# Kernel optimization log

Measured on AMD Instinct MI355X. Metric: run time of the kernel, lower is better.

Reference implementation:

```python
import jax, jax.numpy as jnp
import numpy as np

THRESH = 0.9
NUM_HEADS = 4
HEAD_DIM = 8


def _ln(x, g, b, eps=1e-5):
    m = x.mean(-1, keepdims=True)
    v = ((x - m) ** 2).mean(-1, keepdims=True)
    return (x - m) * jax.lax.rsqrt(v + eps) * g + b


def setup_inputs() -> dict:
    key = jax.random.key(0)
    ks = jax.random.split(key, 32)
    n, d_in, h1, h2, d, ffn, nb = 4096, 512, 128, 64, 32, 64, 2

    def w(k, shape, fan_in):
        return jax.random.normal(k, shape, jnp.float32) * (1.0 / np.sqrt(fan_in))

    inp = {}
    inp["x"] = jax.random.normal(ks[0], (n, d_in), jnp.float32)
    # Autoencoder encoder: input_dim -> 128 -> 64 -> latent_dim
    inp["enc_w1"] = w(ks[1], (d_in, h1), d_in); inp["enc_b1"] = jnp.zeros((h1,), jnp.float32)
    inp["enc_w2"] = w(ks[2], (h1, h2), h1);     inp["enc_b2"] = jnp.zeros((h2,), jnp.float32)
    inp["enc_w3"] = w(ks[3], (h2, d), h2);      inp["enc_b3"] = jnp.zeros((d,), jnp.float32)
    # Transformer blocks (stacked over num_blocks=2)
    inp["wq"] = w(ks[4], (nb, d, d), d); inp["bq"] = jnp.zeros((nb, d), jnp.float32)
    inp["wk"] = w(ks[5], (nb, d, d), d); inp["bk"] = jnp.zeros((nb, d), jnp.float32)
    inp["wv"] = w(ks[6], (nb, d, d), d); inp["bv"] = jnp.zeros((nb, d), jnp.float32)
    inp["wo"] = w(ks[7], (nb, d, d), d); inp["bo"] = jnp.zeros((nb, d), jnp.float32)
    inp["ln1_g"] = jnp.ones((nb, d), jnp.float32);  inp["ln1_b"] = jnp.zeros((nb, d), jnp.float32)
    inp["ffn_w1"] = w(ks[8], (nb, d, ffn), d);      inp["ffn_b1"] = jnp.zeros((nb, ffn), jnp.float32)
    inp["ffn_w2"] = w(ks[9], (nb, ffn, d), ffn);    inp["ffn_b2"] = jnp.zeros((nb, d), jnp.float32)
    inp["ln2_g"] = jnp.ones((nb, d), jnp.float32);  inp["ln2_b"] = jnp.zeros((nb, d), jnp.float32)
    # Head: Linear(d,16) -> Tanh -> Linear(16, num_classes)
    inp["head_w1"] = w(ks[10], (d, 16), d);  inp["head_b1"] = jnp.zeros((16,), jnp.float32)
    inp["head_w2"] = w(ks[11], (16, 1), 16); inp["head_b2"] = jnp.zeros((1,), jnp.float32)
    return inp


def reference(x, enc_w1, enc_b1, enc_w2, enc_b2, enc_w3, enc_b3,
              wq, bq, wk, bk, wv, bv, wo, bo,
              ln1_g, ln1_b, ffn_w1, ffn_b1, ffn_w2, ffn_b2, ln2_g, ln2_b,
              head_w1, head_b1, head_w2, head_b2):
    # --- autoencoder encode: [n, d_in] -> [n, d] ---
    a = jax.nn.relu(x @ enc_w1 + enc_b1)
    a = jax.nn.relu(a @ enc_w2 + enc_b2)
    latent = a @ enc_w3 + enc_b3  # [n, d]

    # --- graph pool: cosine-sim threshold mask, per-node masked neighbor mean ---
    # self-similarity is 1.0 >= THRESH, so every node has >=1 neighbor (deg>=1)
    norms = jnp.linalg.norm(latent, axis=1, keepdims=True) + 1e-12
    normed = latent / norms
    sims = normed @ normed.T                                  # [n, n]
    mask = (sims >= THRESH).astype(latent.dtype)              # [n, n]
    deg = mask.sum(axis=1, keepdims=True)                     # [n, 1]
    pooled = latent + (mask @ latent) / deg                   # latent[i] + mean of neighbors

    # --- transformer blocks (post-LN, eval mode: dropout off) ---
    h = pooled[None]  # [1, n, d]
    n, d = pooled.shape
    nb = wq.shape[0]
    scale = 1.0 / np.sqrt(HEAD_DIM)
    for i in range(nb):
        q = (h @ wq[i] + bq[i]).reshape(1, n, NUM_HEADS, HEAD_DIM)
        k = (h @ wk[i] + bk[i]).reshape(1, n, NUM_HEADS, HEAD_DIM)
        v = (h @ wv[i] + bv[i]).reshape(1, n, NUM_HEADS, HEAD_DIM)
        scores = jnp.einsum('bqhd,bkhd->bhqk', q, k) * scale  # [1, H, n, n]
        attn = jax.nn.softmax(scores, axis=-1)
        o = jnp.einsum('bhqk,bkhd->bqhd', attn, v).reshape(1, n, d)
        o = o @ wo[i] + bo[i]
        h = _ln(h + o, ln1_g[i], ln1_b[i])
        f = jax.nn.relu(h @ ffn_w1[i] + ffn_b1[i]) @ ffn_w2[i] + ffn_b2[i]
        h = _ln(h + f, ln2_g[i], ln2_b[i])

    # --- head on mean-pooled sequence ---
    m = h.mean(axis=1)  # [1, d]
    out = jnp.tanh(m @ head_w1 + head_b1) @ head_w2 + head_b2  # [1, 1]
    return out.squeeze()
```

## Files before the change

### kernel.cpp

```cpp
#include <hip/hip_runtime.h>
#include <math.h>

#define N 4096
#define DIN 512
#define D 32
#define JC 8

typedef float v2f __attribute__((ext_vector_type(2)));
__device__ __forceinline__ v2f fma2(v2f a, float b, v2f c) {
  v2f bb; bb.x = b; bb.y = b;
  return __builtin_elementwise_fma(a, bb, c);
}

__global__ __launch_bounds__(256) void enc_kernel(
    const float* __restrict__ x,
    const float* __restrict__ w1, const float* __restrict__ b1,
    const float* __restrict__ w2, const float* __restrict__ b2,
    const float* __restrict__ w3, const float* __restrict__ b3,
    float* __restrict__ latent, float* __restrict__ normed) {
  __shared__ float xs[8][512];
  __shared__ float h1p[4][8][128];
  __shared__ float h1s[8][128];
  __shared__ float h2s[8][64];
  __shared__ float w2s[128][64];
  __shared__ float w3s[64][32];
  const int t = threadIdx.x;
  const int r0 = blockIdx.x * 8;

  const float4* xg = (const float4*)(x + (size_t)r0 * DIN);
  float4* xl = (float4*)&xs[0][0];
#pragma unroll
  for (int i = 0; i < 4; ++i) xl[t + i * 256] = xg[t + i * 256];
  float4* w2l = (float4*)&w2s[0][0];
  const float4* w2g = (const float4*)w2;
#pragma unroll
  for (int i = 0; i < 8; ++i) w2l[t + i * 256] = w2g[t + i * 256];
  float4* w3l = (float4*)&w3s[0][0];
  const float4* w3g = (const float4*)w3;
#pragma unroll
  for (int i = 0; i < 2; ++i) w3l[t + i * 256] = w3g[t + i * 256];
  __syncthreads();

  {
    const int jc2 = (t & 63) * 2;
    const int kq = t >> 6;
    const int kb = kq * 128;
    float a0[8], a1[8];
#pragma unroll
    for (int r = 0; r < 8; ++r) { a0[r] = 0.f; a1[r] = 0.f; }
    const float* wp = w1 + (size_t)kb * 128 + jc2;

#define ENC_LD4(P0, P1, P2, P3, KK)                          \
    P0 = *(const float2*)&wp[(size_t)(KK) * 128];            \
    P1 = *(const float2*)&wp[(size_t)((KK) + 1) * 128];      \
    P2 = *(const float2*)&wp[(size_t)((KK) + 2) * 128];      \
    P3 = *(const float2*)&wp[(size_t)((KK) + 3) * 128];

#define ENC_STEP(W0, WA, WB, WC, KK)                                   \
    {                                                                  \
      _Pragma("unroll")                                                \
      for (int r = 0; r < 8; ++r) {                                    \
        const float4 xv = *(const float4*)&xs[r][kb + (KK)];           \
        a0[r] = fmaf(xv.x, W0.x, a0[r]); a1[r] = fmaf(xv.x, W0.y, a1[r]); \
        a0[r] = fmaf(xv.y, WA.x, a0[r]); a1[r] = fmaf(xv.y, WA.y, a1[r]); \
        a0[r] = fmaf(xv.z, WB.x, a0[r]); a1[r] = fmaf(xv.z, WB.y, a1[r]); \
        a0[r] = fmaf(xv.w, WC.x, a0[r]); a1[r] = fmaf(xv.w, WC.y, a1[r]); \
      }                                                                \
    }

    float2 A0, A1, A2, A3, B0, B1, B2, B3, C0, C1, C2, C3, D0, D1, D2, D3;
    ENC_LD4(A0, A1, A2, A3, 0)
    ENC_LD4(B0, B1, B2, B3, 4)
    ENC_LD4(C0, C1, C2, C3, 8)
    ENC_LD4(D0, D1, D2, D3, 12)
    for (int kk = 0; kk < 128; kk += 16) {
      ENC_STEP(A0, A1, A2, A3, kk + 0);
      if (kk + 16 < 128) { ENC_LD4(A0, A1, A2, A3, kk + 16) }
      ENC_STEP(B0, B1, B2, B3, kk + 4);
      if (kk + 20 < 128) { ENC_LD4(B0, B1, B2, B3, kk + 20) }
      ENC_STEP(C0, C1, C2, C3, kk + 8);
      if (kk + 24 < 128) { ENC_LD4(C0, C1, C2, C3, kk + 24) }
      ENC_STEP(D0, D1, D2, D3, kk + 12);
      if (kk + 28 < 128) { ENC_LD4(D0, D1, D2, D3, kk + 28) }
    }
#undef ENC_STEP
#undef ENC_LD4
#pragma unroll
    for (int r = 0; r < 8; ++r) {
      h1p[kq][r][jc2] = a0[r];
      h1p[kq][r][jc2 + 1] = a1[r];
    }
  }
  __syncthreads();

#pragma unroll
  for (int e0 = 0; e0 < 1024; e0 += 256) {
    const int e = e0 + t;
    const int r = e >> 7, c = e & 127;
    const float s = b1[c] + ((h1p[0][r][c] + h1p[1][r][c]) + (h1p[2][r][c] + h1p[3][r][c]));
    h1s[r][c] = fmaxf(s, 0.f);
  }
  __syncthreads();

  {
    const int j = t & 63, rg = t >> 6;
    const int ra = rg * 2, rb = ra + 1;
    float a0 = b2[j], a1 = b2[j];
#pragma unroll 8
    for (int kk = 0; kk < 128; ++kk) {
      const float w = w2s[kk][j];
      a0 = fmaf(h1s[ra][kk], w, a0);
      a1 = fmaf(h1s[rb][kk], w, a1);
    }
    h2s[ra][j] = fmaxf(a0, 0.f);
    h2s[rb][j] = fmaxf(a1, 0.f);
  }
  __syncthreads();

  {
    const int j = t & 31, og = t >> 5;
    float acc = b3[j];
#pragma unroll 8
    for (int kk = 0; kk < 64; ++kk) acc = fmaf(h2s[og][kk], w3s[kk][j], acc);
    float s2 = acc * acc;
    s2 += __shfl_xor(s2, 1);
    s2 += __shfl_xor(s2, 2);
    s2 += __shfl_xor(s2, 4);
    s2 += __shfl_xor(s2, 8);
    s2 += __shfl_xor(s2, 16);
    const float inv = 1.0f / (sqrtf(s2) + 1e-12f);
    const size_t off = (size_t)(r0 + og) * D + j;
    latent[off] = acc;
    normed[off] = acc * inv;
  }
}

__global__ __launch_bounds__(256) __attribute__((amdgpu_waves_per_eu(2, 2)))
void pool_kernel(const float* __restrict__ normed,
                 const float* __restrict__ latent,
                 float* __restrict__ pacc,
                 float* __restrict__ pdeg) {
  __shared__ float smem[8192];
  float* nt = smem;
  float* lt = smem + 4096;
  const int t = threadIdx.x;
  const int jg = t & 7, ip = t >> 3;
  const int i0 = blockIdx.x * 64;
  const int j0 = blockIdx.y * 512;

  v2f nip[32];
  {
    const float* nr0 = normed + (size_t)(i0 + ip) * D;
    const float* nr1 = normed + (size_t)(i0 + ip + 32) * D;
#pragma unroll
    for (int c = 0; c < 32; ++c) { nip[c].x = nr0[c]; nip[c].y = nr1[c]; }
  }

  v2f accp[32], deg2;
#pragma unroll
  for (int c = 0; c < 32; ++c) { accp[c].x = 0.f; accp[c].y = 0.f; }
  deg2.x = 0.f; deg2.y = 0.f;

  for (int jt = j0; jt < j0 + 512; jt += 128) {
    __syncthreads();
    const float4* ng = (const float4*)(normed + (size_t)jt * D);
    const float4* lg = (const float4*)(latent + (size_t)jt * D);
    float4* ntl = (float4*)nt;
    float4* ltl = (float4*)lt;
#pragma unroll
    for (int i = 0; i < 4; ++i) {
      const int gidx = t + i * 256;
      const int r = gidx >> 3, cc = gidx & 7, slot = cc ^ (r & 7);
      ntl[r * 8 + slot] = ng[gidx];
      ltl[r * 8 + slot] = lg[gidx];
    }
    __syncthreads();
#pragma unroll 2
    for (int jj = jg; jj < 128; jj += 8) {
      const float4* nr = (const float4*)nt + jj * 8;
      const int sw = jj & 7;
      v2f s2; s2.x = 0.f; s2.y = 0.f;
#pragma unroll
      for (int c4 = 0; c4 < 8; ++c4) {
        const float4 nv = nr[c4 ^ sw];
        s2 = fma2(nip[c4 * 4 + 0], nv.x, s2);
        s2 = fma2(nip[c4 * 4 + 1], nv.y, s2);
        s2 = fma2(nip[c4 * 4 + 2], nv.z, s2);
        s2 = fma2(nip[c4 * 4 + 3], nv.w, s2);
      }
      if (s2.x >= 0.9f || s2.y >= 0.9f) {
        v2f m2;
        m2.x = (s2.x >= 0.9f) ? 1.f : 0.f;
        m2.y = (s2.y >= 0.9f) ? 1.f : 0.f;
        deg2 += m2;
        const float4* lr = (const float4*)lt + jj * 8;
#pragma unroll
        for (int c4 = 0; c4 < 8; ++c4) {
          const float4 lv = lr[c4 ^ sw];
          accp[c4 * 4 + 0] = fma2(m2, lv.x, accp[c4 * 4 + 0]);
          accp[c4 * 4 + 1] = fma2(m2, lv.y, accp[c4 * 4 + 1]);
          accp[c4 * 4 + 2] = fma2(m2, lv.z, accp[c4 * 4 + 2]);
          accp[c4 * 4 + 3] = fma2(m2, lv.w, accp[c4 * 4 + 3]);
        }
      }
    }
  }
#pragma unroll
  for (int m = 1; m <= 4; m <<= 1) {
#pragma unroll
    for (int c = 0; c < 32; ++c) {
      accp[c].x += __shfl_xor(accp[c].x, m);
      accp[c].y += __shfl_xor(accp[c].y, m);
    }
    deg2.x += __shfl_xor(deg2.x, m);
    deg2.y += __shfl_xor(deg2.y, m);
  }
  if (jg == 0) {
    float* pa0 = pacc + ((size_t)blockIdx.y * N + i0 + ip) * 32;
    float* pa1 = pacc + ((size_t)blockIdx.y * N + i0 + ip + 32) * 32;
#pragma unroll
    for (int c = 0; c < 32; ++c) {
      pa0[c] = accp[c].x;
      pa1[c] = accp[c].y;
    }
    pdeg[(size_t)blockIdx.y * N + i0 + ip] = deg2.x;
    pdeg[(size_t)blockIdx.y * N + i0 + ip + 32] = deg2.y;
  }
}

__global__ __launch_bounds__(256) void pool_combine(const float* __restrict__ latent,
                                                    const float* __restrict__ pacc,
                                                    const float* __restrict__ pdeg,
                                                    float* __restrict__ h) {
  const int e = blockIdx.x * 256 + threadIdx.x;
  const int i = e >> 5;
  float s = 0.f, dg = 0.f;
#pragma unroll
  for (int gch = 0; gch < JC; ++gch) {
    s += pacc[(size_t)gch * N * 32 + e];
    dg += pdeg[(size_t)gch * N + i];
  }
  h[e] = latent[e] + s / dg;
}

__global__ __launch_bounds__(256) void qkv_kernel(
    const float* __restrict__ h,
    const float* __restrict__ wq, const float* __restrict__ bq,
    const float* __restrict__ wk, const float* __restrict__ bk,
    const float* __restrict__ wv, const float* __restrict__ bv,
    float* __restrict__ q, float* __restrict__ k, float* __restrict__ v,
    int* __restrict__ kmax2i) {
  __shared__ float hs[32][32];
  __shared__ float wsm[3][32][32];
  __shared__ int kred[4];
  const int t = threadIdx.x;
  const int r0 = blockIdx.x * 32;
  if (t < 4) kred[t] = 0;
  ((float4*)&hs[0][0])[t] = ((const float4*)(h + (size_t)r0 * 32))[t];
  ((float4*)&wsm[0][0][0])[t] = ((const float4*)wq)[t];
  ((float4*)&wsm[1][0][0])[t] = ((const float4*)wk)[t];
  ((float4*)&wsm[2][0][0])[t] = ((const float4*)wv)[t];
  __syncthreads();
  const int j = t & 31, og = t >> 5;
  const int head = j >> 3;
  float aq[4], ak[4], av[4];
#pragma unroll
  for (int u = 0; u < 4; ++u) { aq[u] = bq[j]; ak[u] = bk[j]; av[u] = bv[j]; }
  for (int kk = 0; kk < 32; ++kk) {
    const float wqv = wsm[0][kk][j], wkv = wsm[1][kk][j], wvv = wsm[2][kk][j];
#pragma unroll
    for (int u = 0; u < 4; ++u) {
      const float hh = hs[og * 4 + u][kk];
      aq[u] = fmaf(hh, wqv, aq[u]);
      ak[u] = fmaf(hh, wkv, ak[u]);
      av[u] = fmaf(hh, wvv, av[u]);
    }
  }
  const float scale = 1.4426950408889634f * 0.35355339059327373f;
#pragma unroll
  for (int u = 0; u < 4; ++u) {
    const size_t off = (size_t)(r0 + og * 4 + u) * 32 + j;
    q[off] = aq[u] * scale;
    k[off] = ak[u];
    v[off] = av[u];
  }
#pragma unroll
  for (int u = 0; u < 4; ++u) {
    float s2 = ak[u] * ak[u];
    s2 += __shfl_xor(s2, 1);
    s2 += __shfl_xor(s2, 2);
    s2 += __shfl_xor(s2, 4);
    if ((j & 7) == 0) atomicMax(&kred[head], __float_as_int(s2));
  }
  __syncthreads();
  if (t < 4) atomicMax(&kmax2i[t], kred[t]);
}

__global__ __launch_bounds__(256, 4)
void attn_kernel(const float* __restrict__ q,
                 const float* __restrict__ k,
                 const float* __restrict__ v,
                 const int* __restrict__ kmax2i,
                 float* __restrict__ apacc,
                 float* __restrict__ apl) {
  __shared__ float4 tiles[1024];
  float4* kls = tiles;
  float4* vls = tiles + 512;
  const int t = threadIdx.x;
  const int jg = t & 7, head = (t >> 3) & 3, rg = t >> 5;
  const int r0 = blockIdx.x * 32;
  const int j0 = blockIdx.y * (N / JC);

  const float km2 = __int_as_float(kmax2i[head]);

  v2f qq[2][8], acc[2][8], mneg2[2], l2[2];
#pragma unroll
  for (int pr = 0; pr < 2; ++pr) {
    const float* qr0 = q + (size_t)(r0 + rg * 4 + 2 * pr) * 32 + head * 8;
    const float* qr1 = qr0 + 32;
    const float4 qa0 = ((const float4*)qr0)[0], qb0 = ((const float4*)qr0)[1];
    const float4 qa1 = ((const float4*)qr1)[0], qb1 = ((const float4*)qr1)[1];
    qq[pr][0].x = qa0.x; qq[pr][0].y = qa1.x;
    qq[pr][1].x = qa0.y; qq[pr][1].y = qa1.y;
    qq[pr][2].x = qa0.z; qq[pr][2].y = qa1.z;
    qq[pr][3].x = qa0.w; qq[pr][3].y = qa1.w;
    qq[pr][4].x = qb0.x; qq[pr][4].y = qb1.x;
    qq[pr][5].x = qb0.y; qq[pr][5].y = qb1.y;
    qq[pr][6].x = qb0.z; qq[pr][6].y = qb1.z;
    qq[pr][7].x = qb0.w; qq[pr][7].y = qb1.w;
    const float qn0 = qa0.x * qa0.x + qa0.y * qa0.y + qa0.z * qa0.z + qa0.w * qa0.w +
                      qb0.x * qb0.x + qb0.y * qb0.y + qb0.z * qb0.z + qb0.w * qb0.w;
    const float qn1 = qa1.x * qa1.x + qa1.y * qa1.y + qa1.z * qa1.z + qa1.w * qa1.w +
                      qb1.x * qb1.x + qb1.y * qb1.y + qb1.z * qb1.z + qb1.w * qb1.w;
    mneg2[pr].x = -sqrtf(qn0 * km2);
    mneg2[pr].y = -sqrtf(qn1 * km2);
    l2[pr].x = 0.f; l2[pr].y = 0.f;
#pragma unroll
    for (int c = 0; c < 8; ++c) { acc[pr][c].x = 0.f; acc[pr][c].y = 0.f; }
  }

  float4 kr0, kr1, vr0, vr1;
  {
    const float4* kg = (const float4*)(k + (size_t)j0 * 32);
    const float4* vg = (const float4*)(v + (size_t)j0 * 32);
    kr0 = kg[t]; kr1 = kg[t + 256];
    vr0 = vg[t]; vr1 = vg[t + 256];
  }

  const int rA = t >> 3, slotA = (t & 7) ^ (rA & 7);
  const int g1 = t + 256;
  const int rB = g1 >> 3, slotB = (g1 & 7) ^ (rB & 7);

  const int h2 = head * 2;
  const int s0 = h2 ^ jg, s1 = (h2 + 1) ^ jg;
  for (int jt = j0; jt < j0 + (N / JC); jt += 64) {
    __syncthreads();
    kls[rA * 8 + slotA] = kr0;
    kls[rB * 8 + slotB] = kr1;
    vls[rA * 8 + slotA] = vr0;
    vls[rB * 8 + slotB] = vr1;
    __syncthreads();
    if (jt + 64 < j0 + (N / JC)) {
      const float4* kg = (const float4*)(k + (size_t)(jt + 64) * 32);
      const float4* vg = (const float4*)(v + (size_t)(jt + 64) * 32);
      kr0 = kg[t]; kr1 = kg[t + 256];
      vr0 = vg[t]; vr1 = vg[t + 256];
    }
#pragma unroll 2
    for (int it = 0; it < 8; ++it) {
      const int jj = it * 8 + jg;
      const float4 ka = kls[jj * 8 + s0];
      const float4 kb = kls[jj * 8 + s1];
      const float4 va = vls[jj * 8 + s0];
      const float4 vb = vls[jj * 8 + s1];
#pragma unroll
      for (int pr = 0; pr < 2; ++pr) {
        v2f s2 = mneg2[pr];
        s2 = fma2(qq[pr][0], ka.x, s2);
        s2 = fma2(qq[pr][1], ka.y, s2);
        s2 = fma2(qq[pr][2], ka.z, s2);
        s2 = fma2(qq[pr][3], ka.w, s2);
        s2 = fma2(qq[pr][4], kb.x, s2);
        s2 = fma2(qq[pr][5], kb.y, s2);
        s2 = fma2(qq[pr][6], kb.z, s2);
        s2 = fma2(qq[pr][7], kb.w, s2);
        v2f p2;
        p2.x = __builtin_amdgcn_exp2f(s2.x);
        p2.y = __builtin_amdgcn_exp2f(s2.y);
        l2[pr] += p2;
        acc[pr][0] = fma2(p2, va.x, acc[pr][0]);
        acc[pr][1] = fma2(p2, va.y, acc[pr][1]);
        acc[pr][2] = fma2(p2, va.z, acc[pr][2]);
        acc[pr][3] = fma2(p2, va.w, acc[pr][3]);
        acc[pr][4] = fma2(p2, vb.x, acc[pr][4]);
        acc[pr][5] = fma2(p2, vb.y, acc[pr][5]);
        acc[pr][6] = fma2(p2, vb.z, acc[pr][6]);
        acc[pr][7] = fma2(p2, vb.w, acc[pr][7]);
      }
    }
  }
#pragma unroll
  for (int pr = 0; pr < 2; ++pr) {
#pragma unroll
    for (int m = 1; m <= 4; m <<= 1) {
#pragma unroll
      for (int c = 0; c < 8; ++c) {
        acc[pr][c].x += __shfl_xor(acc[pr][c].x, m);
        acc[pr][c].y += __shfl_xor(acc[pr][c].y, m);
      }
      l2[pr].x += __shfl_xor(l2[pr].x, m);
      l2[pr].y += __shfl_xor(l2[pr].y, m);
    }
  }
  if (jg == 0) {
    const size_t abase = (size_t)blockIdx.y * N * 32;
    const size_t lbase = (size_t)blockIdx.y * N * 4;
#pragma unroll
    for (int pr = 0; pr < 2; ++pr) {
      const int row0 = r0 + rg * 4 + 2 * pr;
      float* ap0 = apacc + abase + (size_t)row0 * 32 + head * 8;
      float* ap1 = ap0 + 32;
#pragma unroll
      for (int c = 0; c < 8; ++c) {
        ap0[c] = acc[pr][c].x;
        ap1[c] = acc[pr][c].y;
      }
      apl[lbase + (size_t)row0 * 4 + head] = l2[pr].x;
      apl[lbase + (size_t)(row0 + 1) * 4 + head] = l2[pr].y;
    }
  }
}

__global__ __launch_bounds__(256) void acombine(const float* __restrict__ apacc,
                                                const float* __restrict__ apl,
                                                float* __restrict__ attno) {
  const int e = blockIdx.x * 256 + threadIdx.x;
  const int row = e >> 5;
  const int hh = (e >> 3) & 3;
  float L = 0.f, S = 0.f;
#pragma unroll
  for (int jc = 0; jc < JC; ++jc) {
    L += apl[(size_t)jc * N * 4 + row * 4 + hh];
    S += apacc[(size_t)jc * N * 32 + e];
  }
  attno[e] = S / L;
}

__global__ __launch_bounds__(256) void oln1_kernel(const float* __restrict__ attno,
                                                   const float* __restrict__ wo,
                                                   const float* __restrict__ bo,
                                                   const float* __restrict__ g,
                                                   const float* __restrict__ b,
                                                   float* __restrict__ h) {
  __shared__ float als[32][32];
  __shared__ float wols[32][32];
  __shared__ float ys[32][33];
  const int t = threadIdx.x;
  const int r0 = blockIdx.x * 32;
  ((float4*)&als[0][0])[t] = ((const float4*)(attno + (size_t)r0 * 32))[t];
  ((float4*)&wols[0][0])[t] = ((const float4*)wo)[t];
  __syncthreads();
  const int j = t & 31, og = t >> 5;
  float acc[4];
#pragma unroll
  for (int u = 0; u < 4; ++u) acc[u] = bo[j];
  for (int kk = 0; kk < 32; ++kk) {
    const float w = wols[kk][j];
#pragma unroll
    for (int u = 0; u < 4; ++u) acc[u] = fmaf(als[og * 4 + u][kk], w, acc[u]);
  }
#pragma unroll
  for (int u = 0; u < 4; ++u) {
    const int r = og * 4 + u;
    ys[r][j] = h[(size_t)(r0 + r) * 32 + j] + acc[u];
  }
  __syncthreads();
  if (t < 32) {
    float mu = 0.f;
#pragma unroll
    for (int c = 0; c < 32; ++c) mu += ys[t][c];
    mu *= (1.f / 32.f);
    float var = 0.f;
#pragma unroll
    for (int c = 0; c < 32; ++c) {
      const float dd = ys[t][c] - mu;
      var = fmaf(dd, dd, var);
    }
    var *= (1.f / 32.f);
    const float rs = rsqrtf(var + 1e-5f);
#pragma unroll
    for (int c = 0; c < 32; ++c)
      h[(size_t)(r0 + t) * 32 + c] = (ys[t][c] - mu) * rs * g[c] + b[c];
  }
}

__global__ __launch_bounds__(256) void ffn_kernel(const float* __restrict__ hin,
                                                  const float* __restrict__ w1,
                                                  const float* __restrict__ b1,
                                                  const float* __restrict__ w2,
                                                  const float* __restrict__ b2,
                                                  const float* __restrict__ g,
                                                  const float* __restrict__ bb,
                                                  float* __restrict__ h) {
  __shared__ float hs[32][32];
  __shared__ float w1s[32][64];
  __shared__ float w2s[64][32];
  __shared__ float mids[32][64];
  __shared__ float ys[32][33];
  const int t = threadIdx.x;
  const int r0 = blockIdx.x * 32;
  ((float4*)&hs[0][0])[t] = ((const float4*)(hin + (size_t)r0 * 32))[t];
#pragma unroll
  for (int i = 0; i < 2; ++i) {
    ((float4*)&w1s[0][0])[t + i * 256] = ((const float4*)w1)[t + i * 256];
    ((float4*)&w2s[0][0])[t + i * 256] = ((const float4*)w2)[t + i * 256];
  }
  __syncthreads();
  {
    const int jm = t & 63, gg = t >> 6;
    float acc[8];
#pragma unroll
    for (int u = 0; u < 8; ++u) acc[u] = b1[jm];
    for (int kk = 0; kk < 32; ++kk) {
      const float w = w1s[kk][jm];
#pragma unroll
      for (int u = 0; u < 8; ++u) acc[u] = fmaf(hs[gg * 8 + u][kk], w, acc[u]);
    }
#pragma unroll
    for (int u = 0; u < 8; ++u) mids[gg * 8 + u][jm] = fmaxf(acc[u], 0.f);
  }
  __syncthreads();
  {
    const int j = t & 31, og = t >> 5;
    float acc[4];
#pragma unroll
    for (int u = 0; u < 4; ++u) acc[u] = b2[j];
    for (int kk = 0; kk < 64; ++kk) {
      const float w = w2s[kk][j];
#pragma unroll
      for (int u = 0; u < 4; ++u) acc[u] = fmaf(mids[og * 4 + u][kk], w, acc[u]);
    }
#pragma unroll
    for (int u = 0; u < 4; ++u) {
      const int r = og * 4 + u;
      ys[r][j] = hs[r][j] + acc[u];
    }
  }
  __syncthreads();
  if (t < 32) {
    float mu = 0.f;
#pragma unroll
    for (int c = 0; c < 32; ++c) mu += ys[t][c];
    mu *= (1.f / 32.f);
    float var = 0.f;
#pragma unroll
    for (int c = 0; c < 32; ++c) {
      const float dd = ys[t][c] - mu;
      var = fmaf(dd, dd, var);
    }
    var *= (1.f / 32.f);
    const float rs = rsqrtf(var + 1e-5f);
#pragma unroll
    for (int c = 0; c < 32; ++c)
      h[(size_t)(r0 + t) * 32 + c] = (ys[t][c] - mu) * rs * g[c] + bb[c];
  }
}

__global__ __launch_bounds__(256) void headp_kernel(const float* __restrict__ h,
                                                    float* __restrict__ partial) {
  __shared__ float red[8][32];
  const int t = threadIdx.x;
  const int c = t & 31, rg = t >> 5;
  const int r0 = blockIdx.x * 64;
  float s = 0.f;
#pragma unroll
  for (int u = 0; u < 8; ++u) s += h[(size_t)(r0 + rg * 8 + u) * 32 + c];
  red[rg][c] = s;
  __syncthreads();
  if (t < 32) {
    float ss = 0.f;
#pragma unroll
    for (int u = 0; u < 8; ++u) ss += red[u][t];
    partial[blockIdx.x * 32 + t] = ss;
  }
}

__global__ __launch_bounds__(64) void headf_kernel(const float* __restrict__ partial,
                                                   const float* __restrict__ w1,
                                                   const float* __restrict__ b1,
                                                   const float* __restrict__ w2,
                                                   const float* __restrict__ b2,
                                                   float* __restrict__ out) {
  __shared__ float mls[32];
  __shared__ float tls[16];
  const int t = threadIdx.x;
  if (t < 32) {
    float s = 0.f;
    for (int bb = 0; bb < 64; ++bb) s += partial[bb * 32 + t];
    mls[t] = s * (1.f / 4096.f);
  }
  __syncthreads();
  if (t < 16) {
    float a = b1[t];
#pragma unroll
    for (int c = 0; c < 32; ++c) a = fmaf(mls[c], w1[c * 16 + t], a);
    tls[t] = tanhf(a);
  }
  __syncthreads();
  if (t == 0) {
    float o = b2[0];
#pragma unroll
    for (int jj = 0; jj < 16; ++jj) o = fmaf(tls[jj], w2[jj], o);
    out[0] = o;
  }
}

extern "C" void kernel_launch(void* const* d_in, const int* in_sizes, int n_in,
                              void* d_out, int out_size, void* d_ws, size_t ws_size,
                              hipStream_t stream) {
  const float* x      = (const float*)d_in[0];
  const float* enc_w1 = (const float*)d_in[1];
  const float* enc_b1 = (const float*)d_in[2];
  const float* enc_w2 = (const float*)d_in[3];
  const float* enc_b2 = (const float*)d_in[4];
  const float* enc_w3 = (const float*)d_in[5];
  const float* enc_b3 = (const float*)d_in[6];
  const float* wq     = (const float*)d_in[7];
  const float* bq     = (const float*)d_in[8];
  const float* wk     = (const float*)d_in[9];
  const float* bk     = (const float*)d_in[10];
  const float* wv     = (const float*)d_in[11];
  const float* bv     = (const float*)d_in[12];
  const float* wo     = (const float*)d_in[13];
  const float* bo     = (const float*)d_in[14];
  const float* ln1_g  = (const float*)d_in[15];
  const float* ln1_b  = (const float*)d_in[16];
  const float* ffn_w1 = (const float*)d_in[17];
  const float* ffn_b1 = (const float*)d_in[18];
  const float* ffn_w2 = (const float*)d_in[19];
  const float* ffn_b2 = (const float*)d_in[20];
  const float* ln2_g  = (const float*)d_in[21];
  const float* ln2_b  = (const float*)d_in[22];
  const float* head_w1 = (const float*)d_in[23];
  const float* head_b1 = (const float*)d_in[24];
  const float* head_w2 = (const float*)d_in[25];
  const float* head_b2 = (const float*)d_in[26];

  float* ws      = (float*)d_ws;
  float* latent  = ws;
  float* normed  = ws + 131072;
  float* h       = ws + 262144;
  float* q       = ws + 393216;
  float* k       = ws + 524288;
  float* v       = ws + 655360;
  float* attno   = ws + 786432;
  float* shreg   = ws + 917504;
  float* p_acc   = shreg;
  float* p_deg   = shreg + 1048576;
  float* a_acc   = shreg;
  float* a_l     = shreg + 1048576;
  int*   kmax2i  = (int*)(ws + 2097152);
  float* partial = ws + 2097216;

  hipMemsetAsync(kmax2i, 0, 8 * sizeof(int), stream);

  enc_kernel<<<512, 256, 0, stream>>>(x, enc_w1, enc_b1, enc_w2, enc_b2, enc_w3, enc_b3,
                                      latent, normed);
  pool_kernel<<<dim3(64, JC), 256, 0, stream>>>(normed, latent, p_acc, p_deg);
  pool_combine<<<512, 256, 0, stream>>>(latent, p_acc, p_deg, h);

  for (int blk = 0; blk < 2; ++blk) {
    qkv_kernel<<<128, 256, 0, stream>>>(h, wq + blk * 1024, bq + blk * 32,
                                        wk + blk * 1024, bk + blk * 32,
                                        wv + blk * 1024, bv + blk * 32, q, k, v,
                                        kmax2i + blk * 4);
    attn_kernel<<<dim3(128, JC), 256, 0, stream>>>(q, k, v, kmax2i + blk * 4, a_acc, a_l);
    acombine<<<512, 256, 0, stream>>>(a_acc, a_l, attno);
    oln1_kernel<<<128, 256, 0, stream>>>(attno, wo + blk * 1024, bo + blk * 32,
                                         ln1_g + blk * 32, ln1_b + blk * 32, h);
    ffn_kernel<<<128, 256, 0, stream>>>(h, ffn_w1 + blk * 2048, ffn_b1 + blk * 64,
                                        ffn_w2 + blk * 2048, ffn_b2 + blk * 32,
                                        ln2_g + blk * 32, ln2_b + blk * 32, h);
  }

  headp_kernel<<<64, 256, 0, stream>>>(h, partial);
  headf_kernel<<<1, 64, 0, stream>>>(partial, head_w1, head_b1, head_w2, head_b2, (float*)d_out);
}
```

Baseline: 171.6 us.

## Fuse split-K combine steps and output-proj/LN/FFN into neighboring kernels

Folds the pooling partial-sum combine into the first qkv kernel, and folds the attention partial combine, the output projection with LN1, and the FFN with LN2 into a single kernel per block. This removes several small launches and the global round trips through the attno and h intermediates. In exchange the fused kernel uses more shared memory per block, which may lower occupancy, and qkv gains a runtime branch.

```diff
diff --git a/kernel.cpp b/kernel.cpp
--- a/kernel.cpp
+++ b/kernel.cpp
@@ -228,35 +228,45 @@
   }
 }
 
-__global__ __launch_bounds__(256) void pool_combine(const float* __restrict__ latent,
-                                                    const float* __restrict__ pacc,
-                                                    const float* __restrict__ pdeg,
-                                                    float* __restrict__ h) {
-  const int e = blockIdx.x * 256 + threadIdx.x;
-  const int i = e >> 5;
-  float s = 0.f, dg = 0.f;
-#pragma unroll
-  for (int gch = 0; gch < JC; ++gch) {
-    s += pacc[(size_t)gch * N * 32 + e];
-    dg += pdeg[(size_t)gch * N + i];
-  }
-  h[e] = latent[e] + s / dg;
-}
-
 __global__ __launch_bounds__(256) void qkv_kernel(
-    const float* __restrict__ h,
+    float* __restrict__ h,
     const float* __restrict__ wq, const float* __restrict__ bq,
     const float* __restrict__ wk, const float* __restrict__ bk,
     const float* __restrict__ wv, const float* __restrict__ bv,
     float* __restrict__ q, float* __restrict__ k, float* __restrict__ v,
-    int* __restrict__ kmax2i) {
+    int* __restrict__ kmax2i,
+    const float* __restrict__ latent,
+    const float* __restrict__ pacc,
+    const float* __restrict__ pdeg,
+    int fuse_combine) {
   __shared__ float hs[32][32];
   __shared__ float wsm[3][32][32];
   __shared__ int kred[4];
   const int t = threadIdx.x;
   const int r0 = blockIdx.x * 32;
   if (t < 4) kred[t] = 0;
-  ((float4*)&hs[0][0])[t] = ((const float4*)(h + (size_t)r0 * 32))[t];
+  if (fuse_combine) {
+    const int el = t * 4;
+    const int gi = r0 + (el >> 5);
+    float4 s4 = make_float4(0.f, 0.f, 0.f, 0.f);
+    float dg = 0.f;
+#pragma unroll
+    for (int jc = 0; jc < JC; ++jc) {
+      const float4 p4 = *(const float4*)&pacc[(size_t)jc * N * 32 + (size_t)r0 * 32 + el];
+      s4.x += p4.x; s4.y += p4.y; s4.z += p4.z; s4.w += p4.w;
+      dg += pdeg[(size_t)jc * N + gi];
+    }
+    const float4 l4 = *(const float4*)&latent[(size_t)r0 * 32 + el];
+    float4 h4;
+    h4.x = l4.x + s4.x / dg;
+    h4.y = l4.y + s4.y / dg;
+    h4.z = l4.z + s4.z / dg;
+    h4.w = l4.w + s4.w / dg;
+    ((float4*)&hs[0][0])[t] = h4;
+    *(float4*)&h[(size_t)r0 * 32 + el] = h4;
+  } else {
+    ((float4*)&hs[0][0])[t] = ((const float4*)(h + (size_t)r0 * 32))[t];
+  }
   ((float4*)&wsm[0][0][0])[t] = ((const float4*)wq)[t];
   ((float4*)&wsm[1][0][0])[t] = ((const float4*)wk)[t];
   ((float4*)&wsm[2][0][0])[t] = ((const float4*)wv)[t];
@@ -431,48 +441,64 @@
   }
 }
 
-__global__ __launch_bounds__(256) void acombine(const float* __restrict__ apacc,
-                                                const float* __restrict__ apl,
-                                                float* __restrict__ attno) {
-  const int e = blockIdx.x * 256 + threadIdx.x;
-  const int row = e >> 5;
-  const int hh = (e >> 3) & 3;
-  float L = 0.f, S = 0.f;
-#pragma unroll
-  for (int jc = 0; jc < JC; ++jc) {
-    L += apl[(size_t)jc * N * 4 + row * 4 + hh];
-    S += apacc[(size_t)jc * N * 32 + e];
-  }
-  attno[e] = S / L;
-}
-
-__global__ __launch_bounds__(256) void oln1_kernel(const float* __restrict__ attno,
-                                                   const float* __restrict__ wo,
-                                                   const float* __restrict__ bo,
-                                                   const float* __restrict__ g,
-                                                   const float* __restrict__ b,
-                                                   float* __restrict__ h) {
+__global__ __launch_bounds__(256) void oln1ffn_kernel(
+    const float* __restrict__ apacc, const float* __restrict__ apl,
+    const float* __restrict__ wo, const float* __restrict__ bo,
+    const float* __restrict__ ln1g, const float* __restrict__ ln1b,
+    const float* __restrict__ w1, const float* __restrict__ b1,
+    const float* __restrict__ w2, const float* __restrict__ b2,
+    const float* __restrict__ ln2g, const float* __restrict__ ln2b,
+    float* __restrict__ h) {
   __shared__ float als[32][32];
   __shared__ float wols[32][32];
+  __shared__ float hs[32][32];
   __shared__ float ys[32][33];
+  __shared__ float w1s[32][64];
+  __shared__ float w2s[64][32];
+  __shared__ float mids[32][64];
   const int t = threadIdx.x;
   const int r0 = blockIdx.x * 32;
-  ((float4*)&als[0][0])[t] = ((const float4*)(attno + (size_t)r0 * 32))[t];
+
+  {
+    const int el = t * 4;
+    const int row = r0 + (el >> 5);
+    const int hh = (el >> 3) & 3;
+    float4 s4 = make_float4(0.f, 0.f, 0.f, 0.f);
+    float L = 0.f;
+#pragma unroll
+    for (int jc = 0; jc < JC; ++jc) {
+      const float4 p4 = *(const float4*)&apacc[(size_t)jc * N * 32 + (size_t)r0 * 32 + el];
+      s4.x += p4.x; s4.y += p4.y; s4.z += p4.z; s4.w += p4.w;
+      L += apl[(size_t)jc * N * 4 + (size_t)row * 4 + hh];
+    }
+    float4 a4;
+    a4.x = s4.x / L; a4.y = s4.y / L; a4.z = s4.z / L; a4.w = s4.w / L;
+    ((float4*)&als[0][0])[t] = a4;
+  }
   ((float4*)&wols[0][0])[t] = ((const float4*)wo)[t];
-  __syncthreads();
+  ((float4*)&hs[0][0])[t] = ((const float4*)(h + (size_t)r0 * 32))[t];
+#pragma unroll
+  for (int i = 0; i < 2; ++i) {
+    ((float4*)&w1s[0][0])[t + i * 256] = ((const float4*)w1)[t + i * 256];
+    ((float4*)&w2s[0][0])[t + i * 256] = ((const float4*)w2)[t + i * 256];
+  }
+  __syncthreads();
+
   const int j = t & 31, og = t >> 5;
-  float acc[4];
-#pragma unroll
-  for (int u = 0; u < 4; ++u) acc[u] = bo[j];
-  for (int kk = 0; kk < 32; ++kk) {
-    const float w = wols[kk][j];
-#pragma unroll
-    for (int u = 0; u < 4; ++u) acc[u] = fmaf(als[og * 4 + u][kk], w, acc[u]);
-  }
-#pragma unroll
-  for (int u = 0; u < 4; ++u) {
-    const int r = og * 4 + u;
-    ys[r][j] = h[(size_t)(r0 + r) * 32 + j] + acc[u];
+  {
+    float acc[4];
+#pragma unroll
+    for (int u = 0; u < 4; ++u) acc[u] = bo[j];
+    for (int kk = 0; kk < 32; ++kk) {
+      const float w = wols[kk][j];
+#pragma unroll
+      for (int u = 0; u < 4; ++u) acc[u] = fmaf(als[og * 4 + u][kk], w, acc[u]);
+    }
+#pragma unroll
+    for (int u = 0; u < 4; ++u) {
+      const int r = og * 4 + u;
+      ys[r][j] = hs[r][j] + acc[u];
+    }
   }
   __syncthreads();
   if (t < 32) {
@@ -490,30 +516,7 @@
     const float rs = rsqrtf(var + 1e-5f);
 #pragma unroll
     for (int c = 0; c < 32; ++c)
-      h[(size_t)(r0 + t) * 32 + c] = (ys[t][c] - mu) * rs * g[c] + b[c];
-  }
-}
-
-__global__ __launch_bounds__(256) void ffn_kernel(const float* __restrict__ hin,
-                                                  const float* __restrict__ w1,
-                                                  const float* __restrict__ b1,
-                                                  const float* __restrict__ w2,
-                                                  const float* __restrict__ b2,
-                                                  const float* __restrict__ g,
-                                                  const float* __restrict__ bb,
-                                                  float* __restrict__ h) {
-  __shared__ float hs[32][32];
-  __shared__ float w1s[32][64];
-  __shared__ float w2s[64][32];
-  __shared__ float mids[32][64];
-  __shared__ float ys[32][33];
-  const int t = threadIdx.x;
-  const int r0 = blockIdx.x * 32;
-  ((float4*)&hs[0][0])[t] = ((const float4*)(hin + (size_t)r0 * 32))[t];
-#pragma unroll
-  for (int i = 0; i < 2; ++i) {
-    ((float4*)&w1s[0][0])[t + i * 256] = ((const float4*)w1)[t + i * 256];
-    ((float4*)&w2s[0][0])[t + i * 256] = ((const float4*)w2)[t + i * 256];
+      als[t][c] = (ys[t][c] - mu) * rs * ln1g[c] + ln1b[c];
   }
   __syncthreads();
   {
@@ -524,14 +527,13 @@
     for (int kk = 0; kk < 32; ++kk) {
       const float w = w1s[kk][jm];
 #pragma unroll
-      for (int u = 0; u < 8; ++u) acc[u] = fmaf(hs[gg * 8 + u][kk], w, acc[u]);
+      for (int u = 0; u < 8; ++u) acc[u] = fmaf(als[gg * 8 + u][kk], w, acc[u]);
     }
 #pragma unroll
     for (int u = 0; u < 8; ++u) mids[gg * 8 + u][jm] = fmaxf(acc[u], 0.f);
   }
   __syncthreads();
   {
-    const int j = t & 31, og = t >> 5;
     float acc[4];
 #pragma unroll
     for (int u = 0; u < 4; ++u) acc[u] = b2[j];
@@ -543,7 +545,7 @@
 #pragma unroll
     for (int u = 0; u < 4; ++u) {
       const int r = og * 4 + u;
-      ys[r][j] = hs[r][j] + acc[u];
+      ys[r][j] = als[r][j] + acc[u];
     }
   }
   __syncthreads();
@@ -562,7 +564,7 @@
     const float rs = rsqrtf(var + 1e-5f);
 #pragma unroll
     for (int c = 0; c < 32; ++c)
-      h[(size_t)(r0 + t) * 32 + c] = (ys[t][c] - mu) * rs * g[c] + bb[c];
+      h[(size_t)(r0 + t) * 32 + c] = (ys[t][c] - mu) * rs * ln2g[c] + ln2b[c];
   }
 }
 
@@ -653,7 +655,6 @@
   float* q       = ws + 393216;
   float* k       = ws + 524288;
   float* v       = ws + 655360;
-  float* attno   = ws + 786432;
   float* shreg   = ws + 917504;
   float* p_acc   = shreg;
   float* p_deg   = shreg + 1048576;
@@ -667,20 +668,20 @@
   enc_kernel<<<512, 256, 0, stream>>>(x, enc_w1, enc_b1, enc_w2, enc_b2, enc_w3, enc_b3,
                                       latent, normed);
   pool_kernel<<<dim3(64, JC), 256, 0, stream>>>(normed, latent, p_acc, p_deg);
-  pool_combine<<<512, 256, 0, stream>>>(latent, p_acc, p_deg, h);
 
   for (int blk = 0; blk < 2; ++blk) {
     qkv_kernel<<<128, 256, 0, stream>>>(h, wq + blk * 1024, bq + blk * 32,
                                         wk + blk * 1024, bk + blk * 32,
                                         wv + blk * 1024, bv + blk * 32, q, k, v,
-                                        kmax2i + blk * 4);
+                                        kmax2i + blk * 4,
+                                        latent, p_acc, p_deg, blk == 0 ? 1 : 0);
     attn_kernel<<<dim3(128, JC), 256, 0, stream>>>(q, k, v, kmax2i + blk * 4, a_acc, a_l);
-    acombine<<<512, 256, 0, stream>>>(a_acc, a_l, attno);
-    oln1_kernel<<<128, 256, 0, stream>>>(attno, wo + blk * 1024, bo + blk * 32,
-                                         ln1_g + blk * 32, ln1_b + blk * 32, h);
-    ffn_kernel<<<128, 256, 0, stream>>>(h, ffn_w1 + blk * 2048, ffn_b1 + blk * 64,
-                                        ffn_w2 + blk * 2048, ffn_b2 + blk * 32,
-                                        ln2_g + blk * 32, ln2_b + blk * 32, h);
+    oln1ffn_kernel<<<128, 256, 0, stream>>>(a_acc, a_l,
+                                            wo + blk * 1024, bo + blk * 32,
+                                            ln1_g + blk * 32, ln1_b + blk * 32,
+                                            ffn_w1 + blk * 2048, ffn_b1 + blk * 64,
+                                            ffn_w2 + blk * 2048, ffn_b2 + blk * 32,
+                                            ln2_g + blk * 32, ln2_b + blk * 32, h);
   }
 
   headp_kernel<<<64, 256, 0, stream>>>(h, partial);
```

New measurement: 160.1 us (median of 2 runs). 6.7% less time.
